# Kernel optimization log

Hardware: AMD Instinct MI355X
Metric: run time of the kernel (lower is better)

The kernel has to match this reference:

```python
import jax, jax.numpy as jnp
import numpy as np

N_NODES = 20000
N_EDGES = 160000
N_GRAPHS = 64
IN_DIM = 1304  # 1280 + 24
NEG_SLOPE = 0.2


def gat_conv(x, src, dst, W, a_src, a_dst, b, heads, out_ch):
    """PyG-style GATConv (source_to_target flow, self loops already appended).
    x: [N, in], W: [in, heads*out], a_src/a_dst: [heads, out], b: [heads*out].
    Returns [N, heads*out] (concat=True)."""
    N = x.shape[0]
    h = (x @ W).reshape(N, heads, out_ch)                 # [N, H, C]
    e_src = jnp.sum(h * a_src[None], axis=-1)             # [N, H]
    e_dst = jnp.sum(h * a_dst[None], axis=-1)             # [N, H]
    e = jax.nn.leaky_relu(e_src[src] + e_dst[dst], NEG_SLOPE)  # [E, H]
    # softmax over incoming edges of each destination node
    e_max = jax.ops.segment_max(e, dst, num_segments=N)   # [N, H]
    e_exp = jnp.exp(e - e_max[dst])
    denom = jax.ops.segment_sum(e_exp, dst, num_segments=N)
    alpha = e_exp / (denom[dst] + 1e-16)                  # [E, H]
    msg = h[src] * alpha[:, :, None]                      # [E, H, C]
    out = jax.ops.segment_sum(msg, dst, num_segments=N)   # [N, H, C]
    return out.reshape(N, heads * out_ch) + b


def setup_inputs() -> dict:
    key = jax.random.key(0)
    ks = jax.random.split(key, 20)
    x = jax.random.normal(ks[0], (N_NODES, IN_DIM), dtype=jnp.float32)
    edge_index = jax.random.randint(ks[1], (2, N_EDGES), 0, N_NODES, dtype=jnp.int32)
    phy = jax.random.normal(ks[2], (N_GRAPHS, 188), dtype=jnp.float32)
    batch = jnp.sort(jax.random.randint(ks[3], (N_NODES,), 0, N_GRAPHS, dtype=jnp.int32))

    def glorot(k, shape):
        fan_in, fan_out = shape[0], shape[-1]
        lim = jnp.sqrt(6.0 / (fan_in + fan_out))
        return jax.random.uniform(k, shape, jnp.float32, -lim, lim)

    params = {
        # conv1: GATConv(1304, 256, heads=3)
        "W1": glorot(ks[4], (IN_DIM, 3 * 256)),
        "a_src1": glorot(ks[5], (3, 256)) * 0.1,
        "a_dst1": glorot(ks[6], (3, 256)) * 0.1,
        "b1": jnp.zeros((3 * 256,), jnp.float32),
        # conv2: GATConv(768, 256, heads=1)
        "W2": glorot(ks[7], (3 * 256, 256)),
        "a_src2": glorot(ks[8], (1, 256)) * 0.1,
        "a_dst2": glorot(ks[9], (1, 256)) * 0.1,
        "b2": jnp.zeros((256,), jnp.float32),
        # fc1
        "fc1_w1": glorot(ks[10], (188, 128)), "fc1_b1": jnp.zeros((128,), jnp.float32),
        "fc1_w2": glorot(ks[11], (128, 128)), "fc1_b2": jnp.zeros((128,), jnp.float32),
        # fc2
        "fc2_w1": glorot(ks[12], (256 + 128, 192)), "fc2_b1": jnp.zeros((192,), jnp.float32),
        "fc2_w2": glorot(ks[13], (192, 2)), "fc2_b2": jnp.zeros((2,), jnp.float32),
    }
    return {"x": x, "edge_index": edge_index, "phy": phy, "batch": batch, **params}


def reference(x, edge_index, phy, batch,
              W1, a_src1, a_dst1, b1,
              W2, a_src2, a_dst2, b2,
              fc1_w1, fc1_b1, fc1_w2, fc1_b2,
              fc2_w1, fc2_b1, fc2_w2, fc2_b2):
    N = x.shape[0]
    # add self loops (PyG GATConv default)
    loops = jnp.arange(N, dtype=edge_index.dtype)
    src = jnp.concatenate([edge_index[0], loops])
    dst = jnp.concatenate([edge_index[1], loops])

    h = gat_conv(x, src, dst, W1, a_src1, a_dst1, b1, heads=3, out_ch=256)
    h = jax.nn.relu(h)  # dropout is identity at inference
    h = gat_conv(h, src, dst, W2, a_src2, a_dst2, b2, heads=1, out_ch=256)

    # global mean pool per graph
    sums = jax.ops.segment_sum(h, batch, num_segments=N_GRAPHS)        # [B, 256]
    cnts = jax.ops.segment_sum(jnp.ones((N,), h.dtype), batch, num_segments=N_GRAPHS)
    pooled = sums / jnp.maximum(cnts, 1.0)[:, None]

    mid = jax.nn.relu(phy @ fc1_w1 + fc1_b1)
    mid = jax.nn.relu(mid @ fc1_w2 + fc1_b2)

    z = jnp.concatenate([pooled, mid], axis=1)                          # [B, 384]
    z = jax.nn.relu(z @ fc2_w1 + fc2_b1)
    logits = z @ fc2_w2 + fc2_b2
    return jax.nn.softmax(logits, axis=1)
```

## Files before the change

kernel.cpp:

```cpp
#include <hip/hip_runtime.h>
#include <hip/hip_bf16.h>
#include <math.h>

#define NN    20000
#define MP1   20224
#define NP    20096
#define E0    160000
#define EL    180000
#define NG    64
#define INDIM 1304
#define K1P   1344
#define GNT   21
#define GNX   3
#define GMB   79
#define NEG_SLOPE 0.2f
#define PCH   8
#define NSB   20

typedef __bf16 bf16x8 __attribute__((ext_vector_type(8)));
typedef __bf16 bf16x4 __attribute__((ext_vector_type(4)));
typedef float  f32x4  __attribute__((ext_vector_type(4)));

__device__ __forceinline__ void gload16(const void* g, void* l) {
    __builtin_amdgcn_global_load_lds(
        (const __attribute__((address_space(1))) void*)g,
        (__attribute__((address_space(3))) void*)l, 16, 0, 0);
}

#define BAR()  { __builtin_amdgcn_s_barrier(); asm volatile("" ::: "memory"); }
#define VMW(n) { asm volatile("s_waitcnt vmcnt(" #n ")" ::: "memory"); __builtin_amdgcn_sched_barrier(0); }

__device__ __forceinline__ void stA(const __hip_bfloat16* __restrict__ A, int bm, int kt, int mh,
                                    char* abuf, int w, int l) {
#pragma unroll
    for (int u = 0; u < 2; u++) {
        int rl = (w << 3) + (l >> 3);
        int lrow = u * 128 + mh * 64 + rl;
        int skb = ((l & 7) << 4) ^ ((rl & 7) << 4);
        const char* g = (const char*)(A + (size_t)(bm + lrow) * K1P + kt * 64) + skb;
        gload16(g, abuf + (u * 128 + mh * 64) * 128 + (w << 10));
    }
}

__device__ __forceinline__ void stB(const __hip_bfloat16* __restrict__ Bt, int bn, int kt, int nh,
                                    char* bbuf, int w, int l) {
#pragma unroll
    for (int u = 0; u < 2; u++) {
        int c = u * 2 + (w >> 2);
        int row0 = c * 64 + nh * 32;
        int rl = ((w & 3) << 3) + (l >> 3);
        int skb = ((l & 7) << 4) ^ ((rl & 7) << 4);
        const char* g = (const char*)(Bt + (size_t)(bn + row0 + rl) * K1P + kt * 64) + skb;
        gload16(g, bbuf + row0 * 128 + ((w & 3) << 10));
    }
}

__global__ __launch_bounds__(512)
void gemm256(const __hip_bfloat16* __restrict__ A,
             const __hip_bfloat16* __restrict__ Bt,
             __hip_bfloat16* __restrict__ C,
             const float* __restrict__ a_src, const float* __restrict__ a_dst,
             float* __restrict__ esrc, float* __restrict__ edst, int M) {
    __shared__ char lds[131072];
    const int t = threadIdx.x;
    const int w = t >> 6, l = t & 63;
    const int wm = w >> 2, wn = w & 3;
    const int fr = l & 15, fq = l >> 4;
    const int amask = (fr & 7) << 4;

    const int nwg = GMB * GNX;
    const int q8 = nwg >> 3, r8 = nwg & 7;
    const int xcd = blockIdx.x & 7, sub = blockIdx.x >> 3;
    const int logical = (xcd < r8 ? xcd * (q8 + 1) : r8 * (q8 + 1) + (xcd - r8) * q8) + sub;
    const int bm = (logical / GNX) * 256;
    const int bn = (logical % GNX) * 256;

    f32x4 acc[8][4];
#pragma unroll
    for (int i = 0; i < 8; i++)
#pragma unroll
        for (int j = 0; j < 4; j++) acc[i][j] = (f32x4){0.f, 0.f, 0.f, 0.f};

    char* A0 = lds;            char* B0 = lds + 32768;
    char* A1 = lds + 65536;    char* B1 = lds + 98304;

    stA(A, bm, 0, 0, A0, w, l);
    stB(Bt, bn, 0, 0, B0, w, l);
    stA(A, bm, 0, 1, A0, w, l);
    stB(Bt, bn, 0, 1, B0, w, l);
    stA(A, bm, 1, 0, A1, w, l);
    stB(Bt, bn, 1, 0, B1, w, l);
    VMW(8);
    BAR();

    for (int kt = 0; kt < GNT; kt++) {
        char* Ab = lds + (kt & 1) * 65536;
        char* Bb = Ab + 32768;
        char* An = lds + ((kt + 1) & 1) * 65536;
        char* Bn = An + 32768;
        bf16x8 a_c[4][2], b_c0[2][2], b_c1[2][2];

#pragma unroll
        for (int im = 0; im < 4; im++)
#pragma unroll
            for (int kk = 0; kk < 2; kk++)
                a_c[im][kk] = *(const bf16x8*)(Ab + (wm * 128 + im * 16 + fr) * 128 + ((kk * 64 + fq * 16) ^ amask));
#pragma unroll
        for (int jn = 0; jn < 2; jn++)
#pragma unroll
            for (int kk = 0; kk < 2; kk++)
                b_c0[jn][kk] = *(const bf16x8*)(Bb + (wn * 64 + jn * 16 + fr) * 128 + ((kk * 64 + fq * 16) ^ amask));
        if (kt + 1 < GNT) stA(A, bm, kt + 1, 1, An, w, l);
        BAR();
        __builtin_amdgcn_s_setprio(1);
#pragma unroll
        for (int im = 0; im < 4; im++)
#pragma unroll
            for (int jn = 0; jn < 2; jn++)
#pragma unroll
                for (int kk = 0; kk < 2; kk++)
                    acc[im][jn] = __builtin_amdgcn_mfma_f32_16x16x32_bf16(a_c[im][kk], b_c0[jn][kk], acc[im][jn], 0, 0, 0);
        __builtin_amdgcn_s_setprio(0);
        if (kt == GNT - 1) { VMW(0); } else { VMW(6); }
        BAR();

#pragma unroll
        for (int jn = 0; jn < 2; jn++)
#pragma unroll
            for (int kk = 0; kk < 2; kk++)
                b_c1[jn][kk] = *(const bf16x8*)(Bb + (wn * 64 + 32 + jn * 16 + fr) * 128 + ((kk * 64 + fq * 16) ^ amask));
        if (kt + 1 < GNT) stB(Bt, bn, kt + 1, 1, Bn, w, l);
        BAR();
        __builtin_amdgcn_s_setprio(1);
#pragma unroll
        for (int im = 0; im < 4; im++)
#pragma unroll
            for (int jn = 0; jn < 2; jn++)
#pragma unroll
                for (int kk = 0; kk < 2; kk++)
                    acc[im][2 + jn] = __builtin_amdgcn_mfma_f32_16x16x32_bf16(a_c[im][kk], b_c1[jn][kk], acc[im][2 + jn], 0, 0, 0);
        __builtin_amdgcn_s_setprio(0);
        if (kt == GNT - 1) { VMW(2); } else { VMW(10); }
        BAR();

#pragma unroll
        for (int im = 0; im < 4; im++)
#pragma unroll
            for (int kk = 0; kk < 2; kk++)
                a_c[im][kk] = *(const bf16x8*)(Ab + (wm * 128 + 64 + im * 16 + fr) * 128 + ((kk * 64 + fq * 16) ^ amask));
        if (kt + 2 < GNT) stA(A, bm, kt + 2, 0, Ab, w, l);
        BAR();
        __builtin_amdgcn_s_setprio(1);
#pragma unroll
        for (int im = 0; im < 4; im++)
#pragma unroll
            for (int jn = 0; jn < 2; jn++)
#pragma unroll
                for (int kk = 0; kk < 2; kk++)
                    acc[4 + im][jn] = __builtin_amdgcn_mfma_f32_16x16x32_bf16(a_c[im][kk], b_c0[jn][kk], acc[4 + im][jn], 0, 0, 0);
        __builtin_amdgcn_s_setprio(0);
        BAR();

        if (kt + 2 < GNT) stB(Bt, bn, kt + 2, 0, Bb, w, l);
        BAR();
        __builtin_amdgcn_s_setprio(1);
#pragma unroll
        for (int im = 0; im < 4; im++)
#pragma unroll
            for (int jn = 0; jn < 2; jn++)
#pragma unroll
                for (int kk = 0; kk < 2; kk++)
                    acc[4 + im][2 + jn] = __builtin_amdgcn_mfma_f32_16x16x32_bf16(a_c[im][kk], b_c1[jn][kk], acc[4 + im][2 + jn], 0, 0, 0);
        __builtin_amdgcn_s_setprio(0);
        if (kt + 2 < GNT) { VMW(8); }
        else if (kt + 2 == GNT) { VMW(4); }
        BAR();
    }

#pragma unroll
    for (int i = 0; i < 8; i++)
#pragma unroll
        for (int j = 0; j < 4; j++)
#pragma unroll
            for (int r = 0; r < 4; r++) {
                int row = bm + wm * 128 + i * 16 + fq * 4 + r;
                int col = bn + wn * 64 + j * 16 + fr;
                if (row < M) C[(size_t)row * 768 + col] = __float2bfloat16(acc[i][j][r]);
            }

    const int head = bn >> 8;
    float asv[4], adv[4];
#pragma unroll
    for (int j = 0; j < 4; j++) {
        asv[j] = a_src[head * 256 + wn * 64 + j * 16 + fr];
        adv[j] = a_dst[head * 256 + wn * 64 + j * 16 + fr];
    }
    __syncthreads();
    float* eb = (float*)lds;
#pragma unroll
    for (int i = 0; i < 8; i++) {
#pragma unroll
        for (int r = 0; r < 4; r++) {
            float ps = 0.f, pd = 0.f;
#pragma unroll
            for (int j = 0; j < 4; j++) { ps += acc[i][j][r] * asv[j]; pd += acc[i][j][r] * adv[j]; }
#pragma unroll
            for (int o = 8; o >= 1; o >>= 1) { ps += __shfl_xor(ps, o, 64); pd += __shfl_xor(pd, o, 64); }
            if (fr == 0) {
                int rowl = wm * 128 + i * 16 + fq * 4 + r;
                eb[(rowl * 4 + wn) * 2 + 0] = ps;
                eb[(rowl * 4 + wn) * 2 + 1] = pd;
            }
        }
    }
    __syncthreads();
    if (t < 256) {
        int row = bm + t;
        if (row < M) {
            float s = eb[t * 8 + 0] + eb[t * 8 + 2] + eb[t * 8 + 4] + eb[t * 8 + 6];
            float d = eb[t * 8 + 1] + eb[t * 8 + 3] + eb[t * 8 + 5] + eb[t * 8 + 7];
            esrc[row * 3 + head] = s;
            edst[row * 3 + head] = d;
        }
    }
}

template<typename CT>
__global__ __launch_bounds__(256)
void mfma_gemm(const __hip_bfloat16* __restrict__ A,
               const __hip_bfloat16* __restrict__ Bt,
               CT* __restrict__ C,
               int M, int N, int K, int NX) {
    __shared__ __hip_bfloat16 As[2][128 * 32];
    __shared__ __hip_bfloat16 Bs[2][128 * 32];
    const int t = threadIdx.x;
    const int w = t >> 6;
    const int l = t & 63;

    const int nwg = gridDim.x;
    const int q = nwg >> 3, r = nwg & 7;
    const int xcd = blockIdx.x & 7, idx = blockIdx.x >> 3;
    const int logical = (xcd < r ? xcd * (q + 1) : r * (q + 1) + (xcd - r) * q) + idx;
    const int bm = (logical / NX) * 128;
    const int bn = (logical % NX) * 128;

    const int wm = (w >> 1) * 64;
    const int wn = (w & 1) * 64;

    f32x4 acc[4][4];
#pragma unroll
    for (int i = 0; i < 4; i++)
#pragma unroll
        for (int j = 0; j < 4; j++) acc[i][j] = (f32x4){0.f, 0.f, 0.f, 0.f};

    const int sr = t >> 2;
    const int sc = (t & 3) * 8;
    const __hip_bfloat16* a0 = A  + (size_t)(bm + sr)      * K + sc;
    const __hip_bfloat16* a1 = A  + (size_t)(bm + 64 + sr) * K + sc;
    const __hip_bfloat16* b0 = Bt + (size_t)(bn + sr)      * K + sc;
    const __hip_bfloat16* b1 = Bt + (size_t)(bn + 64 + sr) * K + sc;

    const int fr = l & 15;
    const int fq = l >> 4;
    const int NT = K / 32;

    auto stage = [&](int k0, int b) {
        char* asb = (char*)&As[b][0];
        char* bsb = (char*)&Bs[b][0];
        gload16(a0 + k0, asb + w * 1024);
        gload16(a1 + k0, asb + 4096 + w * 1024);
        gload16(b0 + k0, bsb + w * 1024);
        gload16(b1 + k0, bsb + 4096 + w * 1024);
    };

    stage(0, 0);
    __syncthreads();

    for (int kt = 0; kt < NT; kt++) {
        const int cb = kt & 1;
        if (kt + 1 < NT) stage((kt + 1) * 32, cb ^ 1);
        bf16x8 av[4], bv[4];
#pragma unroll
        for (int i = 0; i < 4; i++)
            av[i] = *(const bf16x8*)&As[cb][(wm + i * 16 + fr) * 32 + fq * 8];
#pragma unroll
        for (int j = 0; j < 4; j++)
            bv[j] = *(const bf16x8*)&Bs[cb][(wn + j * 16 + fr) * 32 + fq * 8];
#pragma unroll
        for (int i = 0; i < 4; i++)
#pragma unroll
            for (int j = 0; j < 4; j++)
                acc[i][j] = __builtin_amdgcn_mfma_f32_16x16x32_bf16(av[i], bv[j], acc[i][j], 0, 0, 0);
        __syncthreads();
    }

#pragma unroll
    for (int i = 0; i < 4; i++) {
#pragma unroll
        for (int j = 0; j < 4; j++) {
#pragma unroll
            for (int r2 = 0; r2 < 4; r2++) {
                int row = bm + wm + i * 16 + fq * 4 + r2;
                int col = bn + wn + j * 16 + fr;
                if (row < M) {
                    if constexpr (sizeof(CT) == 2)
                        C[(size_t)row * N + col] = __float2bfloat16(acc[i][j][r2]);
                    else
                        C[(size_t)row * N + col] = acc[i][j][r2];
                }
            }
        }
    }
}

__global__ __launch_bounds__(256)
void convert_x(const float* __restrict__ X, __hip_bfloat16* __restrict__ Xb) {
    int idx = blockIdx.x * 256 + threadIdx.x;
    const int nb = K1P / 8;
    if (idx >= MP1 * nb) return;
    int row = idx / nb;
    int cb = (idx - row * nb) * 8;
    union { __hip_bfloat16 h[8]; float4 f4; } u;
    if (row < NN && cb + 8 <= INDIM) {
        const float4* p = (const float4*)(X + (size_t)row * INDIM + cb);
        float4 u0 = p[0], u1 = p[1];
        u.h[0] = __float2bfloat16(u0.x); u.h[1] = __float2bfloat16(u0.y);
        u.h[2] = __float2bfloat16(u0.z); u.h[3] = __float2bfloat16(u0.w);
        u.h[4] = __float2bfloat16(u1.x); u.h[5] = __float2bfloat16(u1.y);
        u.h[6] = __float2bfloat16(u1.z); u.h[7] = __float2bfloat16(u1.w);
    } else {
#pragma unroll
        for (int e = 0; e < 8; e++) {
            float f = (row < NN && cb + e < INDIM) ? X[(size_t)row * INDIM + cb + e] : 0.f;
            u.h[e] = __float2bfloat16(f);
        }
    }
    *(float4*)(Xb + (size_t)row * K1P + cb) = u.f4;
}

__global__ __launch_bounds__(256)
void convert_w_all(const float* __restrict__ W1, const float* __restrict__ W2,
                   __hip_bfloat16* __restrict__ w1t, __hip_bfloat16* __restrict__ w2t) {
    int idx = blockIdx.x * 256 + threadIdx.x;
    const int n1 = 768 * K1P;
    if (idx < n1) {
        int n = idx / K1P, k = idx - n * K1P;
        float f = (k < INDIM) ? W1[(size_t)k * 768 + n] : 0.f;
        w1t[idx] = __float2bfloat16(f);
    } else {
        int i2 = idx - n1;
        if (i2 < 256 * 768) {
            int n = i2 / 768, k = i2 - n * 768;
            w2t[i2] = __float2bfloat16(W2[(size_t)k * 256 + n]);
        }
    }
}

template<int H>
__global__ __launch_bounds__(256)
void compute_e(const __hip_bfloat16* __restrict__ hfeat, const float* __restrict__ a_src,
               const float* __restrict__ a_dst, float* __restrict__ esrc,
               float* __restrict__ edst, int N) {
    const int wv = threadIdx.x >> 6, lane = threadIdx.x & 63;
    const int n = blockIdx.x * 4 + wv;
    if (n >= N) return;
#pragma unroll
    for (int hd = 0; hd < H; hd++) {
        bf16x4 hv = *(const bf16x4*)(hfeat + (size_t)n * (H * 256) + hd * 256 + lane * 4);
        float ps = 0.f, pd = 0.f;
#pragma unroll
        for (int e = 0; e < 4; e++) {
            float f = (float)hv[e];
            ps += f * a_src[hd * 256 + lane * 4 + e];
            pd += f * a_dst[hd * 256 + lane * 4 + e];
        }
#pragma unroll
        for (int o = 32; o > 0; o >>= 1) {
            ps += __shfl_down(ps, o, 64);
            pd += __shfl_down(pd, o, 64);
        }
        if (lane == 0) {
            esrc[n * H + hd] = ps;
            edst[n * H + hd] = pd;
        }
    }
}

__global__ void hist_kernel(const int* __restrict__ ei, int* __restrict__ deg) {
    int e = blockIdx.x * 256 + threadIdx.x;
    if (e >= EL) return;
    int d = (e < E0) ? ei[E0 + e] : (e - E0);
    atomicAdd(&deg[d], 1);
}

__global__ __launch_bounds__(1024)
void scan_blk(const int* __restrict__ deg, int* __restrict__ off, int* __restrict__ bsum) {
    __shared__ int wsum[16];
    const int b = blockIdx.x, t = threadIdx.x, lane = t & 63, wv = t >> 6;
    const int i = b * 1024 + t;
    int v = (i < NN) ? deg[i] : 0;
    int x = v;
#pragma unroll
    for (int o = 1; o < 64; o <<= 1) {
        int y = __shfl_up(x, o, 64);
        if (lane >= o) x += y;
    }
    if (lane == 63) wsum[wv] = x;
    __syncthreads();
    if (wv == 0 && lane < 16) {
        int s = wsum[lane];
#pragma unroll
        for (int o = 1; o < 16; o <<= 1) {
            int y = __shfl_up(s, o, 64);
            if (lane >= o) s += y;
        }
        wsum[lane] = s;
    }
    __syncthreads();
    int woff = (wv == 0) ? 0 : wsum[wv - 1];
    if (i < NN) off[i + 1] = woff + x;
    if (t == 1023) bsum[b] = wsum[15];
}

__global__ void scan_top(const int* __restrict__ bsum, int* __restrict__ boff) {
    int lane = threadIdx.x;
    int v = (lane < NSB) ? bsum[lane] : 0;
    int x = v;
#pragma unroll
    for (int o = 1; o < 64; o <<= 1) {
        int y = __shfl_up(x, o, 64);
        if (lane >= o) x += y;
    }
    if (lane < NSB) boff[lane] = x - v;
}

__global__ __launch_bounds__(1024)
void scan_add(int* __restrict__ off, const int* __restrict__ boff) {
    const int b = blockIdx.x, t = threadIdx.x;
    const int i = b * 1024 + t;
    if (i < NN) off[i + 1] += boff[b];
    if (b == 0 && t == 0) off[0] = 0;
}

__global__ void fill_kernel(const int* __restrict__ ei, const int* __restrict__ off,
                            int* __restrict__ cur, int* __restrict__ csr) {
    int e = blockIdx.x * 256 + threadIdx.x;
    if (e >= EL) return;
    int d = (e < E0) ? ei[E0 + e] : (e - E0);
    int s = (e < E0) ? ei[e] : (e - E0);
    int pos = off[d] + atomicAdd(&cur[d], 1);
    csr[pos] = s;
}

template<int H, bool RELU, typename OutT>
__global__ __launch_bounds__(256)
void gat_aggregate(const __hip_bfloat16* __restrict__ hfeat,
                   const float* __restrict__ esrc,
                   const float* __restrict__ edst,
                   const int* __restrict__ off, const int* __restrict__ csr,
                   const float* __restrict__ bias,
                   OutT* __restrict__ out, int N) {
    const int wv = threadIdx.x >> 6, lane = threadIdx.x & 63;
    const int n = blockIdx.x * 4 + wv;
    if (n >= N) return;
    const int beg = off[n];
    const int deg = off[n + 1] - beg;

    float ed[H], m[H], den[H];
    f32x4 acc[H];
#pragma unroll
    for (int h = 0; h < H; h++) {
        ed[h] = edst[n * H + h];
        m[h] = -INFINITY;
        den[h] = 0.f;
        acc[h] = (f32x4){0.f, 0.f, 0.f, 0.f};
    }

    for (int base = 0; base < deg; base += 64) {
        const int i = base + lane;
        int s = 0;
        float lg[H];
        if (i < deg) {
            s = csr[beg + i];
#pragma unroll
            for (int h = 0; h < H; h++) {
                float v = esrc[s * H + h] + ed[h];
                lg[h] = (v >= 0.f) ? v : NEG_SLOPE * v;
            }
        } else {
#pragma unroll
            for (int h = 0; h < H; h++) lg[h] = -INFINITY;
        }
        float cm[H];
#pragma unroll
        for (int h = 0; h < H; h++) {
            cm[h] = lg[h];
#pragma unroll
            for (int o = 1; o < 64; o <<= 1)
                cm[h] = fmaxf(cm[h], __shfl_xor(cm[h], o, 64));
        }
#pragma unroll
        for (int h = 0; h < H; h++) {
            float nm = fmaxf(m[h], cm[h]);
            float sc = expf(m[h] - nm);
            den[h] *= sc;
#pragma unroll
            for (int e = 0; e < 4; e++) acc[h][e] *= sc;
            m[h] = nm;
        }
        float wgt[H];
#pragma unroll
        for (int h = 0; h < H; h++) {
            wgt[h] = (i < deg) ? expf(lg[h] - m[h]) : 0.f;
            den[h] += wgt[h];
        }
        const int cnt = min(64, deg - base);
        for (int j = 0; j < cnt; j++) {
            int sj = __shfl(s, j, 64);
#pragma unroll
            for (int h = 0; h < H; h++) {
                float wj = __shfl(wgt[h], j, 64);
                bf16x4 hv = *(const bf16x4*)(hfeat + (size_t)sj * (H * 256) + h * 256 + 4 * lane);
#pragma unroll
                for (int e = 0; e < 4; e++) acc[h][e] += wj * (float)hv[e];
            }
        }
    }
#pragma unroll
    for (int h = 0; h < H; h++) {
#pragma unroll
        for (int o = 1; o < 64; o <<= 1) den[h] += __shfl_xor(den[h], o, 64);
    }
#pragma unroll
    for (int h = 0; h < H; h++) {
        float inv = 1.f / (den[h] + 1e-16f);
        if constexpr (sizeof(OutT) == 2) {
            bf16x4 r;
#pragma unroll
            for (int e = 0; e < 4; e++) {
                float f = acc[h][e] * inv + bias[h * 256 + 4 * lane + e];
                if (RELU) f = fmaxf(f, 0.f);
                r[e] = (__bf16)f;
            }
            *(bf16x4*)((__hip_bfloat16*)out + (size_t)n * (H * 256) + h * 256 + 4 * lane) = r;
        } else {
            float4 r;
            float* rp = &r.x;
#pragma unroll
            for (int e = 0; e < 4; e++) {
                float f = acc[h][e] * inv + bias[h * 256 + 4 * lane + e];
                if (RELU) f = fmaxf(f, 0.f);
                rp[e] = f;
            }
            *(float4*)((float*)out + (size_t)n * (H * 256) + h * 256 + 4 * lane) = r;
        }
    }
}

__device__ __forceinline__ int lower_bound_batch(const int* __restrict__ batch, int key) {
    int lo = 0, hi = NN;
    while (lo < hi) {
        int mid = (lo + hi) >> 1;
        if (batch[mid] < key) lo = mid + 1; else hi = mid;
    }
    return lo;
}

__global__ __launch_bounds__(256)
void pool_partial(const float* __restrict__ out2, const int* __restrict__ batch,
                  float* __restrict__ partial, float* __restrict__ cnts) {
    const int g = blockIdx.x, c = blockIdx.y, t = threadIdx.x;
    const int s = lower_bound_batch(batch, g);
    const int e = lower_bound_batch(batch, g + 1);
    float acc = 0.f;
    for (int n = s + c; n < e; n += PCH) acc += out2[(size_t)n * 256 + t];
    partial[((size_t)g * PCH + c) * 256 + t] = acc;
    if (t == 0 && c == 0) cnts[g] = (float)(e - s);
}

__global__ __launch_bounds__(256)
void head_kernel(const float* __restrict__ phy, const float* __restrict__ partial,
                 const float* __restrict__ cnts,
                 const float* __restrict__ w11, const float* __restrict__ b11,
                 const float* __restrict__ w12, const float* __restrict__ b12,
                 const float* __restrict__ w21, const float* __restrict__ b21,
                 const float* __restrict__ w22, const float* __restrict__ b22,
                 float* __restrict__ out) {
    int g = blockIdx.x, t = threadIdx.x;
    __shared__ float ph[188];
    __shared__ float z[384];
    __shared__ float mid[128];
    __shared__ float t1[192];
    __shared__ float lg[2];
    if (t < 188) ph[t] = phy[g * 188 + t];
    {
        float s = 0.f;
#pragma unroll
        for (int c = 0; c < PCH; c++) s += partial[((size_t)g * PCH + c) * 256 + t];
        z[t] = s / fmaxf(cnts[g], 1.0f);
    }
    __syncthreads();
    if (t < 128) {
        float s = b11[t];
        for (int k = 0; k < 188; k++) s += ph[k] * w11[k * 128 + t];
        mid[t] = fmaxf(s, 0.f);
    }
    __syncthreads();
    if (t < 128) {
        float s = b12[t];
        for (int k = 0; k < 128; k++) s += mid[k] * w12[k * 128 + t];
        z[256 + t] = fmaxf(s, 0.f);
    }
    __syncthreads();
    if (t < 192) {
        float s = b21[t];
        for (int k = 0; k < 384; k++) s += z[k] * w21[k * 192 + t];
        t1[t] = fmaxf(s, 0.f);
    }
    __syncthreads();
    if (t < 2) {
        float s = b22[t];
        for (int k = 0; k < 192; k++) s += t1[k] * w22[k * 2 + t];
        lg[t] = s;
    }
    __syncthreads();
    if (t == 0) {
        float mx = fmaxf(lg[0], lg[1]);
        float e0 = expf(lg[0] - mx), e1 = expf(lg[1] - mx);
        float d = e0 + e1;
        out[g * 2 + 0] = e0 / d;
        out[g * 2 + 1] = e1 / d;
    }
}

extern "C" void kernel_launch(void* const* d_in, const int* in_sizes, int n_in,
                              void* d_out, int out_size, void* d_ws, size_t ws_size,
                              hipStream_t stream) {
    const float* x       = (const float*)d_in[0];
    const int*   ei      = (const int*)  d_in[1];
    const float* phy     = (const float*)d_in[2];
    const int*   batch   = (const int*)  d_in[3];
    const float* W1      = (const float*)d_in[4];
    const float* a_src1  = (const float*)d_in[5];
    const float* a_dst1  = (const float*)d_in[6];
    const float* b1      = (const float*)d_in[7];
    const float* W2      = (const float*)d_in[8];
    const float* a_src2  = (const float*)d_in[9];
    const float* a_dst2  = (const float*)d_in[10];
    const float* b2      = (const float*)d_in[11];
    const float* fc1_w1  = (const float*)d_in[12];
    const float* fc1_b1  = (const float*)d_in[13];
    const float* fc1_w2  = (const float*)d_in[14];
    const float* fc1_b2  = (const float*)d_in[15];
    const float* fc2_w1  = (const float*)d_in[16];
    const float* fc2_b1  = (const float*)d_in[17];
    const float* fc2_w2  = (const float*)d_in[18];
    const float* fc2_b2  = (const float*)d_in[19];
    float* out = (float*)d_out;

    char* base = (char*)d_ws;
    size_t o = 0;
    auto alloc = [&](size_t bytes) { size_t r = o; o += (bytes + 255) & ~255ULL; return r; };

    size_t o_xb   = alloc((size_t)MP1 * K1P * 2);
    size_t o_w1t  = alloc((size_t)768 * K1P * 2);
    size_t o_w2t  = alloc((size_t)256 * 768 * 2);
    size_t o_h1b  = alloc((size_t)NP * 768 * 2);
    size_t o_hob  = alloc((size_t)NP * 768 * 2);
    size_t o_es1  = alloc((size_t)NN * 3 * 4);
    size_t o_ed1  = alloc((size_t)NN * 3 * 4);
    size_t o_es2  = alloc((size_t)NN * 4);
    size_t o_ed2  = alloc((size_t)NN * 4);
    size_t o_deg  = alloc((size_t)(NN + 1) * 4);
    size_t o_cur  = alloc((size_t)NN * 4);
    size_t o_off  = alloc((size_t)(NN + 1) * 4);
    size_t o_csr  = alloc((size_t)EL * 4);
    size_t o_bsum = alloc((size_t)NSB * 4);
    size_t o_boff = alloc((size_t)NSB * 4);
    size_t o_part = alloc((size_t)NG * PCH * 256 * 4);
    size_t o_cnts = alloc((size_t)NG * 4);

    __hip_bfloat16* xb   = (__hip_bfloat16*)(base + o_xb);
    __hip_bfloat16* w1t  = (__hip_bfloat16*)(base + o_w1t);
    __hip_bfloat16* w2t  = (__hip_bfloat16*)(base + o_w2t);
    __hip_bfloat16* h1b  = (__hip_bfloat16*)(base + o_h1b);
    __hip_bfloat16* hob  = (__hip_bfloat16*)(base + o_hob);
    __hip_bfloat16* h2b  = (__hip_bfloat16*)(base + o_xb);
    float*          out2 = (float*)(base + o_xb + (size_t)24 * 1024 * 1024);
    float* es1   = (float*)(base + o_es1);
    float* ed1   = (float*)(base + o_ed1);
    float* es2   = (float*)(base + o_es2);
    float* ed2   = (float*)(base + o_ed2);
    int*   deg   = (int*)(base + o_deg);
    int*   cur   = (int*)(base + o_cur);
    int*   offs  = (int*)(base + o_off);
    int*   csr   = (int*)(base + o_csr);
    int*   bsum  = (int*)(base + o_bsum);
    int*   boff  = (int*)(base + o_boff);
    float* part  = (float*)(base + o_part);
    float* cnts  = (float*)(base + o_cnts);

    hipMemsetAsync(deg, 0, (o_cur - o_deg) + (size_t)NN * 4, stream);
    hipMemsetAsync(hob + (size_t)NN * 768, 0, (size_t)(NP - NN) * 768 * 2, stream);

    convert_x<<<(MP1 * (K1P / 8) + 255) / 256, 256, 0, stream>>>(x, xb);
    convert_w_all<<<(768 * K1P + 256 * 768 + 255) / 256, 256, 0, stream>>>(W1, W2, w1t, w2t);

    hist_kernel<<<(EL + 255) / 256, 256, 0, stream>>>(ei, deg);
    scan_blk<<<NSB, 1024, 0, stream>>>(deg, offs, bsum);
    scan_top<<<1, 64, 0, stream>>>(bsum, boff);
    scan_add<<<NSB, 1024, 0, stream>>>(offs, boff);
    fill_kernel<<<(EL + 255) / 256, 256, 0, stream>>>(ei, offs, cur, csr);

    gemm256<<<GMB * GNX, 512, 0, stream>>>(xb, w1t, h1b, a_src1, a_dst1, es1, ed1, NN);
    gat_aggregate<3, true, __hip_bfloat16><<<(NN + 3) / 4, 256, 0, stream>>>(h1b, es1, ed1, offs, csr, b1, hob, NN);

    mfma_gemm<__hip_bfloat16><<<2 * 157, 256, 0, stream>>>(hob, w2t, h2b, NN, 256, 768, 2);
    compute_e<1><<<(NN + 3) / 4, 256, 0, stream>>>(h2b, a_src2, a_dst2, es2, ed2, NN);
    gat_aggregate<1, false, float><<<(NN + 3) / 4, 256, 0, stream>>>(h2b, es2, ed2, offs, csr, b2, out2, NN);

    pool_partial<<<dim3(NG, PCH), 256, 0, stream>>>(out2, batch, part, cnts);
    head_kernel<<<NG, 256, 0, stream>>>(phy, part, cnts,
                                        fc1_w1, fc1_b1, fc1_w2, fc1_b2,
                                        fc2_w1, fc2_b1, fc2_w2, fc2_b2, out);
}
```

Baseline: 255.0 us.

## Fuse init kernels, merge attention logits into GEMM2 epilogue, bf16 layer-2 output

Folds the two memsets and the X and W bf16 conversions into one block-partitioned init kernel. Folds the scan_top pass into scan_add. Replaces the separate compute_e pass with a GEMM2 epilogue that reduces the accumulator against a_src/a_dst and atomically adds per-row partial logits. Stores the layer-2 aggregation output in bf16 for pooling. The aim is to cut kernel launches and an extra read of h2, in exchange for atomics on the logit buffers and some loss of precision in the pooled features.

```diff
diff --git a/kernel.cpp b/kernel.cpp
--- a/kernel.cpp
+++ b/kernel.cpp
@@ -17,6 +17,10 @@
 #define PCH   8
 #define NSB   20
 
+#define ZB    80
+#define XB    13272
+#define WB    4800
+
 typedef __bf16 bf16x8 __attribute__((ext_vector_type(8)));
 typedef __bf16 bf16x4 __attribute__((ext_vector_type(4)));
 typedef float  f32x4  __attribute__((ext_vector_type(4)));
@@ -29,6 +33,57 @@
 
 #define BAR()  { __builtin_amdgcn_s_barrier(); asm volatile("" ::: "memory"); }
 #define VMW(n) { asm volatile("s_waitcnt vmcnt(" #n ")" ::: "memory"); __builtin_amdgcn_sched_barrier(0); }
+
+__global__ __launch_bounds__(256)
+void init_kernel(uint4* __restrict__ zreg, int n16,
+                 const float* __restrict__ X, __hip_bfloat16* __restrict__ Xb,
+                 const float* __restrict__ W1, const float* __restrict__ W2,
+                 __hip_bfloat16* __restrict__ w1t, __hip_bfloat16* __restrict__ w2t) {
+    const int b = blockIdx.x, t = threadIdx.x;
+    if (b < ZB) {
+        int i = b * 256 + t;
+        if (i < n16) zreg[i] = (uint4){0u, 0u, 0u, 0u};
+        return;
+    }
+    if (b < ZB + XB) {
+        int idx = (b - ZB) * 256 + t;
+        const int nb = K1P / 8;
+        int row = idx / nb;
+        int cb = (idx - row * nb) * 8;
+        union { __hip_bfloat16 h[8]; float4 f4; } u;
+        if (row < NN && cb + 8 <= INDIM) {
+            const float4* p = (const float4*)(X + (size_t)row * INDIM + cb);
+            float4 u0 = p[0], u1 = p[1];
+            u.h[0] = __float2bfloat16(u0.x); u.h[1] = __float2bfloat16(u0.y);
+            u.h[2] = __float2bfloat16(u0.z); u.h[3] = __float2bfloat16(u0.w);
+            u.h[4] = __float2bfloat16(u1.x); u.h[5] = __float2bfloat16(u1.y);
+            u.h[6] = __float2bfloat16(u1.z); u.h[7] = __float2bfloat16(u1.w);
+        } else {
+#pragma unroll
+            for (int e = 0; e < 8; e++) {
+                float f = (row < NN && cb + e < INDIM) ? X[(size_t)row * INDIM + cb + e] : 0.f;
+                u.h[e] = __float2bfloat16(f);
+            }
+        }
+        *(float4*)(Xb + (size_t)row * K1P + cb) = u.f4;
+        return;
+    }
+    {
+        int idx = (b - ZB - XB) * 256 + t;
+        const int n1 = 768 * K1P;
+        if (idx < n1) {
+            int n = idx / K1P, k = idx - n * K1P;
+            float f = (k < INDIM) ? W1[(size_t)k * 768 + n] : 0.f;
+            w1t[idx] = __float2bfloat16(f);
+        } else {
+            int i2 = idx - n1;
+            if (i2 < 256 * 768) {
+                int n = i2 / 768, k = i2 - n * 768;
+                w2t[i2] = __float2bfloat16(W2[(size_t)k * 256 + n]);
+            }
+        }
+    }
+}
 
 __device__ __forceinline__ void stA(const __hip_bfloat16* __restrict__ A, int bm, int kt, int mh,
                                     char* abuf, int w, int l) {
@@ -225,12 +280,13 @@
     }
 }
 
-template<typename CT>
 __global__ __launch_bounds__(256)
-void mfma_gemm(const __hip_bfloat16* __restrict__ A,
-               const __hip_bfloat16* __restrict__ Bt,
-               CT* __restrict__ C,
-               int M, int N, int K, int NX) {
+void gemm2_fused(const __hip_bfloat16* __restrict__ A,
+                 const __hip_bfloat16* __restrict__ Bt,
+                 __hip_bfloat16* __restrict__ C,
+                 const float* __restrict__ a_src2, const float* __restrict__ a_dst2,
+                 float* __restrict__ esrc, float* __restrict__ edst,
+                 int M, int N, int K, int NX) {
     __shared__ __hip_bfloat16 As[2][128 * 32];
     __shared__ __hip_bfloat16 Bs[2][128 * 32];
     const int t = threadIdx.x;
@@ -302,86 +358,42 @@
             for (int r2 = 0; r2 < 4; r2++) {
                 int row = bm + wm + i * 16 + fq * 4 + r2;
                 int col = bn + wn + j * 16 + fr;
-                if (row < M) {
-                    if constexpr (sizeof(CT) == 2)
-                        C[(size_t)row * N + col] = __float2bfloat16(acc[i][j][r2]);
-                    else
-                        C[(size_t)row * N + col] = acc[i][j][r2];
-                }
-            }
-        }
-    }
-}
-
-__global__ __launch_bounds__(256)
-void convert_x(const float* __restrict__ X, __hip_bfloat16* __restrict__ Xb) {
-    int idx = blockIdx.x * 256 + threadIdx.x;
-    const int nb = K1P / 8;
-    if (idx >= MP1 * nb) return;
-    int row = idx / nb;
-    int cb = (idx - row * nb) * 8;
-    union { __hip_bfloat16 h[8]; float4 f4; } u;
-    if (row < NN && cb + 8 <= INDIM) {
-        const float4* p = (const float4*)(X + (size_t)row * INDIM + cb);
-        float4 u0 = p[0], u1 = p[1];
-        u.h[0] = __float2bfloat16(u0.x); u.h[1] = __float2bfloat16(u0.y);
-        u.h[2] = __float2bfloat16(u0.z); u.h[3] = __float2bfloat16(u0.w);
-        u.h[4] = __float2bfloat16(u1.x); u.h[5] = __float2bfloat16(u1.y);
-        u.h[6] = __float2bfloat16(u1.z); u.h[7] = __float2bfloat16(u1.w);
-    } else {
-#pragma unroll
-        for (int e = 0; e < 8; e++) {
-            float f = (row < NN && cb + e < INDIM) ? X[(size_t)row * INDIM + cb + e] : 0.f;
-            u.h[e] = __float2bfloat16(f);
-        }
-    }
-    *(float4*)(Xb + (size_t)row * K1P + cb) = u.f4;
-}
-
-__global__ __launch_bounds__(256)
-void convert_w_all(const float* __restrict__ W1, const float* __restrict__ W2,
-                   __hip_bfloat16* __restrict__ w1t, __hip_bfloat16* __restrict__ w2t) {
-    int idx = blockIdx.x * 256 + threadIdx.x;
-    const int n1 = 768 * K1P;
-    if (idx < n1) {
-        int n = idx / K1P, k = idx - n * K1P;
-        float f = (k < INDIM) ? W1[(size_t)k * 768 + n] : 0.f;
-        w1t[idx] = __float2bfloat16(f);
-    } else {
-        int i2 = idx - n1;
-        if (i2 < 256 * 768) {
-            int n = i2 / 768, k = i2 - n * 768;
-            w2t[i2] = __float2bfloat16(W2[(size_t)k * 256 + n]);
-        }
-    }
-}
-
-template<int H>
-__global__ __launch_bounds__(256)
-void compute_e(const __hip_bfloat16* __restrict__ hfeat, const float* __restrict__ a_src,
-               const float* __restrict__ a_dst, float* __restrict__ esrc,
-               float* __restrict__ edst, int N) {
-    const int wv = threadIdx.x >> 6, lane = threadIdx.x & 63;
-    const int n = blockIdx.x * 4 + wv;
-    if (n >= N) return;
-#pragma unroll
-    for (int hd = 0; hd < H; hd++) {
-        bf16x4 hv = *(const bf16x4*)(hfeat + (size_t)n * (H * 256) + hd * 256 + lane * 4);
-        float ps = 0.f, pd = 0.f;
-#pragma unroll
-        for (int e = 0; e < 4; e++) {
-            float f = (float)hv[e];
-            ps += f * a_src[hd * 256 + lane * 4 + e];
-            pd += f * a_dst[hd * 256 + lane * 4 + e];
-        }
-#pragma unroll
-        for (int o = 32; o > 0; o >>= 1) {
-            ps += __shfl_down(ps, o, 64);
-            pd += __shfl_down(pd, o, 64);
-        }
-        if (lane == 0) {
-            esrc[n * H + hd] = ps;
-            edst[n * H + hd] = pd;
+                if (row < M) C[(size_t)row * N + col] = __float2bfloat16(acc[i][j][r2]);
+            }
+        }
+    }
+
+    float asv[4], adv[4];
+#pragma unroll
+    for (int j = 0; j < 4; j++) {
+        asv[j] = a_src2[bn + wn + j * 16 + fr];
+        adv[j] = a_dst2[bn + wn + j * 16 + fr];
+    }
+    __syncthreads();
+    float* eb = (float*)&As[0][0];
+#pragma unroll
+    for (int i = 0; i < 4; i++) {
+#pragma unroll
+        for (int r2 = 0; r2 < 4; r2++) {
+            float ps = 0.f, pd = 0.f;
+#pragma unroll
+            for (int j = 0; j < 4; j++) { ps += acc[i][j][r2] * asv[j]; pd += acc[i][j][r2] * adv[j]; }
+#pragma unroll
+            for (int o = 8; o >= 1; o >>= 1) { ps += __shfl_xor(ps, o, 64); pd += __shfl_xor(pd, o, 64); }
+            if (fr == 0) {
+                int rowl = wm + i * 16 + fq * 4 + r2;
+                int wnIdx = wn >> 6;
+                eb[(rowl * 2 + wnIdx) * 2 + 0] = ps;
+                eb[(rowl * 2 + wnIdx) * 2 + 1] = pd;
+            }
+        }
+    }
+    __syncthreads();
+    if (t < 128) {
+        int row = bm + t;
+        if (row < M) {
+            atomicAdd(&esrc[row], eb[t * 4 + 0] + eb[t * 4 + 2]);
+            atomicAdd(&edst[row], eb[t * 4 + 1] + eb[t * 4 + 3]);
         }
     }
 }
@@ -422,23 +434,24 @@
     if (t == 1023) bsum[b] = wsum[15];
 }
 
-__global__ void scan_top(const int* __restrict__ bsum, int* __restrict__ boff) {
-    int lane = threadIdx.x;
-    int v = (lane < NSB) ? bsum[lane] : 0;
-    int x = v;
-#pragma unroll
-    for (int o = 1; o < 64; o <<= 1) {
-        int y = __shfl_up(x, o, 64);
-        if (lane >= o) x += y;
-    }
-    if (lane < NSB) boff[lane] = x - v;
-}
-
 __global__ __launch_bounds__(1024)
-void scan_add(int* __restrict__ off, const int* __restrict__ boff) {
+void scan_add(int* __restrict__ off, const int* __restrict__ bsum) {
+    __shared__ int boffs[NSB];
     const int b = blockIdx.x, t = threadIdx.x;
+    if (t < 64) {
+        int lane = t;
+        int v = (lane < NSB) ? bsum[lane] : 0;
+        int x = v;
+#pragma unroll
+        for (int o = 1; o < 64; o <<= 1) {
+            int y = __shfl_up(x, o, 64);
+            if (lane >= o) x += y;
+        }
+        if (lane < NSB) boffs[lane] = x - v;
+    }
+    __syncthreads();
     const int i = b * 1024 + t;
-    if (i < NN) off[i + 1] += boff[b];
+    if (i < NN) off[i + 1] += boffs[b];
     if (b == 0 && t == 0) off[0] = 0;
 }
 
@@ -567,13 +580,13 @@
 }
 
 __global__ __launch_bounds__(256)
-void pool_partial(const float* __restrict__ out2, const int* __restrict__ batch,
+void pool_partial(const __hip_bfloat16* __restrict__ out2, const int* __restrict__ batch,
                   float* __restrict__ partial, float* __restrict__ cnts) {
     const int g = blockIdx.x, c = blockIdx.y, t = threadIdx.x;
     const int s = lower_bound_batch(batch, g);
     const int e = lower_bound_batch(batch, g + 1);
     float acc = 0.f;
-    for (int n = s + c; n < e; n += PCH) acc += out2[(size_t)n * 256 + t];
+    for (int n = s + c; n < e; n += PCH) acc += __bfloat162float(out2[(size_t)n * 256 + t]);
     partial[((size_t)g * PCH + c) * 256 + t] = acc;
     if (t == 0 && c == 0) cnts[g] = (float)(e - s);
 }
@@ -673,12 +686,13 @@
     size_t o_ed2  = alloc((size_t)NN * 4);
     size_t o_deg  = alloc((size_t)(NN + 1) * 4);
     size_t o_cur  = alloc((size_t)NN * 4);
+    size_t o_zend = o;
     size_t o_off  = alloc((size_t)(NN + 1) * 4);
     size_t o_csr  = alloc((size_t)EL * 4);
     size_t o_bsum = alloc((size_t)NSB * 4);
-    size_t o_boff = alloc((size_t)NSB * 4);
     size_t o_part = alloc((size_t)NG * PCH * 256 * 4);
     size_t o_cnts = alloc((size_t)NG * 4);
+    (void)o_cnts;
 
     __hip_bfloat16* xb   = (__hip_bfloat16*)(base + o_xb);
     __hip_bfloat16* w1t  = (__hip_bfloat16*)(base + o_w1t);
@@ -686,7 +700,7 @@
     __hip_bfloat16* h1b  = (__hip_bfloat16*)(base + o_h1b);
     __hip_bfloat16* hob  = (__hip_bfloat16*)(base + o_hob);
     __hip_bfloat16* h2b  = (__hip_bfloat16*)(base + o_xb);
-    float*          out2 = (float*)(base + o_xb + (size_t)24 * 1024 * 1024);
+    __hip_bfloat16* out2 = (__hip_bfloat16*)(base + o_xb + (size_t)24 * 1024 * 1024);
     float* es1   = (float*)(base + o_es1);
     float* ed1   = (float*)(base + o_ed1);
     float* es2   = (float*)(base + o_es2);
@@ -696,28 +710,25 @@
     int*   offs  = (int*)(base + o_off);
     int*   csr   = (int*)(base + o_csr);
     int*   bsum  = (int*)(base + o_bsum);
-    int*   boff  = (int*)(base + o_boff);
     float* part  = (float*)(base + o_part);
     float* cnts  = (float*)(base + o_cnts);
 
-    hipMemsetAsync(deg, 0, (o_cur - o_deg) + (size_t)NN * 4, stream);
-    hipMemsetAsync(hob + (size_t)NN * 768, 0, (size_t)(NP - NN) * 768 * 2, stream);
-
-    convert_x<<<(MP1 * (K1P / 8) + 255) / 256, 256, 0, stream>>>(x, xb);
-    convert_w_all<<<(768 * K1P + 256 * 768 + 255) / 256, 256, 0, stream>>>(W1, W2, w1t, w2t);
+    {
+        int n16 = (int)((o_zend - o_es2) / 16);
+        init_kernel<<<ZB + XB + WB, 256, 0, stream>>>((uint4*)(base + o_es2), n16,
+                                                      x, xb, W1, W2, w1t, w2t);
+    }
 
     hist_kernel<<<(EL + 255) / 256, 256, 0, stream>>>(ei, deg);
     scan_blk<<<NSB, 1024, 0, stream>>>(deg, offs, bsum);
-    scan_top<<<1, 64, 0, stream>>>(bsum, boff);
-    scan_add<<<NSB, 1024, 0, stream>>>(offs, boff);
+    scan_add<<<NSB, 1024, 0, stream>>>(offs, bsum);
     fill_kernel<<<(EL + 255) / 256, 256, 0, stream>>>(ei, offs, cur, csr);
 
     gemm256<<<GMB * GNX, 512, 0, stream>>>(xb, w1t, h1b, a_src1, a_dst1, es1, ed1, NN);
     gat_aggregate<3, true, __hip_bfloat16><<<(NN + 3) / 4, 256, 0, stream>>>(h1b, es1, ed1, offs, csr, b1, hob, NN);
 
-    mfma_gemm<__hip_bfloat16><<<2 * 157, 256, 0, stream>>>(hob, w2t, h2b, NN, 256, 768, 2);
-    compute_e<1><<<(NN + 3) / 4, 256, 0, stream>>>(h2b, a_src2, a_dst2, es2, ed2, NN);
-    gat_aggregate<1, false, float><<<(NN + 3) / 4, 256, 0, stream>>>(h2b, es2, ed2, offs, csr, b2, out2, NN);
+    gemm2_fused<<<2 * 157, 256, 0, stream>>>(hob, w2t, h2b, a_src2, a_dst2, es2, ed2, NN, 256, 768, 2);
+    gat_aggregate<1, false, __hip_bfloat16><<<(NN + 3) / 4, 256, 0, stream>>>(h2b, es2, ed2, offs, csr, b2, out2, NN);
 
     pool_partial<<<dim3(NG, PCH), 256, 0, stream>>>(out2, batch, part, cnts);
     head_kernel<<<NG, 256, 0, stream>>>(phy, part, cnts,
```

Result: faster. 243.5 us (-4.5%).
